# Kernel tuning notes

Measured on AMD Instinct MI355X. Metric: run time of the kernel, lower is better.

The kernel has to match this reference:

```python
import jax, jax.numpy as jnp
import numpy as np

D_MODEL = 1024
H = 16
D_K = D_MODEL // H
NEG_INF = -1.0e9  # matches masked_fill value in the torch source


def setup_inputs() -> dict:
    key = jax.random.key(0)
    kq, kk, kv, kwq, kwk, kwv, kwo = jax.random.split(key, 7)
    B, S = 2, 2048
    query = jax.random.normal(kq, (B, S, D_MODEL), dtype=jnp.float32)
    key_t = jax.random.normal(kk, (B, S, D_MODEL), dtype=jnp.float32)
    value = jax.random.normal(kv, (B, S, D_MODEL), dtype=jnp.float32)
    # causal mask: 1 = attend, 0 = masked (masked_fill(mask == 0, -1e9))
    masked_val = jnp.tril(jnp.ones((S, S), dtype=jnp.int32))[None, None, :, :]
    scale = 1.0 / np.sqrt(D_MODEL)
    w_q = jax.random.normal(kwq, (D_MODEL, D_MODEL), dtype=jnp.float32) * scale
    w_k = jax.random.normal(kwk, (D_MODEL, D_MODEL), dtype=jnp.float32) * scale
    w_v = jax.random.normal(kwv, (D_MODEL, D_MODEL), dtype=jnp.float32) * scale
    w_o = jax.random.normal(kwo, (D_MODEL, D_MODEL), dtype=jnp.float32) * scale
    return {"query": query, "key": key_t, "value": value, "masked_val": masked_val,
            "w_q": w_q, "w_k": w_k, "w_v": w_v, "w_o": w_o}


def reference(query, key, value, masked_val, w_q, w_k, w_v, w_o):
    B, Sq, _ = query.shape
    Sk = key.shape[1]
    # nn.Linear(x) = x @ W.T; weights stored as [out, in]
    Q = (query @ w_q.T).reshape(B, Sq, H, D_K).transpose(0, 2, 1, 3)  # [B,H,Sq,Dk]
    K = (key @ w_k.T).reshape(B, Sk, H, D_K).transpose(0, 2, 1, 3)    # [B,H,Sk,Dk]
    V = (value @ w_v.T).reshape(B, Sk, H, D_K).transpose(0, 2, 1, 3)  # [B,H,Sk,Dk]
    scores = jnp.einsum("bhqd,bhkd->bhqk", Q, K) / jnp.sqrt(jnp.float32(D_K))
    scores = jnp.where(masked_val == 0, NEG_INF, scores)
    probs = jax.nn.softmax(scores, axis=-1)  # dropout p=0.0 -> identity
    ctx = jnp.einsum("bhqk,bhkd->bhqd", probs, V)  # [B,H,Sq,Dk]
    ctx = ctx.transpose(0, 2, 1, 3).reshape(B, Sq, H * D_K)
    return ctx @ w_o.T
```

## Files before the change

### kernel.cpp

```cpp
#include <hip/hip_runtime.h>
#include <hip/hip_bf16.h>
#include <type_traits>

using bf16x8_t = __attribute__((ext_vector_type(8))) __bf16;
using f32x4_t  = __attribute__((ext_vector_type(4))) float;

#define MFMA16(a, b, c) __builtin_amdgcn_mfma_f32_16x16x32_bf16((a), (b), (c), 0, 0, 0)

constexpr int BATCH   = 2;
constexpr int SEQ     = 2048;
constexpr int DMODEL  = 1024;
constexpr int DK      = 64;
constexpr int MTOT    = BATCH * SEQ;
constexpr float SCL2 = 0.125f * 1.44269504088896f;

typedef const __attribute__((address_space(1))) unsigned int ga_u32;
typedef __attribute__((address_space(3))) unsigned int ls_u32;
__device__ __forceinline__ void glds16(const void* g, void* l) {
    __builtin_amdgcn_global_load_lds((ga_u32*)g, (ls_u32*)l, 16, 0, 0);
}

__device__ __forceinline__ float exp2_fast(float x) {
    float r;
    asm volatile("v_exp_f32 %0, %1" : "=v"(r) : "v"(x));
    return r;
}

__device__ __forceinline__ bf16x8_t cvt8(const float* __restrict__ p) {
    f32x4_t a = *(const f32x4_t*)p;
    f32x4_t b = *(const f32x4_t*)(p + 4);
    bf16x8_t r;
    r[0] = (__bf16)a[0]; r[1] = (__bf16)a[1]; r[2] = (__bf16)a[2]; r[3] = (__bf16)a[3];
    r[4] = (__bf16)b[0]; r[5] = (__bf16)b[1]; r[6] = (__bf16)b[2]; r[7] = (__bf16)b[3];
    return r;
}

__global__ __launch_bounds__(256) void cvt_all_kernel(
    const float* __restrict__ q, const float* __restrict__ k, const float* __restrict__ v,
    const float* __restrict__ w0, const float* __restrict__ w1,
    const float* __restrict__ w2, const float* __restrict__ w3,
    __bf16* __restrict__ dstA, __bf16* __restrict__ dstW)
{
    const int y = blockIdx.y;
    const float* src;
    __bf16* dst;
    if (y < 3) {
        const float* a[3] = {q, k, v};
        src = a[y];
        dst = dstA + (size_t)y * (MTOT * DMODEL);
    } else {
        if (blockIdx.x >= 512) return;
        const float* w[4] = {w0, w1, w2, w3};
        src = w[y - 3];
        dst = dstW + (size_t)(y - 3) * (DMODEL * DMODEL);
    }
    size_t i = ((size_t)blockIdx.x * 256 + threadIdx.x) * 8;
    *(bf16x8_t*)(dst + i) = cvt8(src + i);
}

template<bool C_F32>
__device__ __forceinline__ void gemm_body(
    const __bf16* __restrict__ A, const __bf16* __restrict__ Bt,
    void* __restrict__ Cp, int m0, int n0, float cscale)
{
    constexpr int K = DMODEL, N = DMODEL;
    constexpr int NS = K / 32;
    __shared__ __align__(16) char smem[3][16384];

    const int tid  = threadIdx.x;
    const int wave = tid >> 6, lane = tid & 63;
    const int wm = wave >> 1, wn = wave & 1;
    const int l15 = lane & 15, lhi = lane >> 4;

    auto stage = [&](int k0, int buf) {
        #pragma unroll
        for (int i = 0; i < 2; ++i) {
            int cbase = i * 256 + wave * 64;
            int slot = cbase + lane;
            int row = slot >> 2, c = slot & 3;
            int cs = (c + 4 - ((row >> 1) & 3)) & 3;
            glds16(A + (size_t)(m0 + row) * K + k0 + cs * 8, smem[buf] + (size_t)cbase * 16);
        }
        #pragma unroll
        for (int i = 0; i < 2; ++i) {
            int cbase = i * 256 + wave * 64;
            int slot = cbase + lane;
            int row = slot >> 2, c = slot & 3;
            int cs = (c + 4 - ((row >> 1) & 3)) & 3;
            glds16(Bt + (size_t)(n0 + row) * K + k0 + cs * 8,
                   smem[buf] + 8192 + (size_t)cbase * 16);
        }
    };

    f32x4_t acc[4][4] = {};

    auto mfma_step = [&](int buf) {
        const __bf16* a_ls = (const __bf16*)smem[buf];
        const __bf16* b_ls = (const __bf16*)(smem[buf] + 8192);
        bf16x8_t af[4], bfr[4];
        #pragma unroll
        for (int i = 0; i < 4; ++i) {
            int row = wm * 64 + i * 16 + l15;
            int lc = (lhi + (row >> 1)) & 3;
            af[i] = *(const bf16x8_t*)(a_ls + row * 32 + lc * 8);
        }
        #pragma unroll
        for (int j = 0; j < 4; ++j) {
            int row = wn * 64 + j * 16 + l15;
            int lc = (lhi + (row >> 1)) & 3;
            bfr[j] = *(const bf16x8_t*)(b_ls + row * 32 + lc * 8);
        }
        #pragma unroll
        for (int i = 0; i < 4; ++i)
            #pragma unroll
            for (int j = 0; j < 4; ++j)
                acc[i][j] = MFMA16(af[i], bfr[j], acc[i][j]);
    };

    stage(0, 0);
    stage(32, 1);

    for (int t = 0; t < NS - 2; ++t) {
        asm volatile("s_waitcnt vmcnt(4)" ::: "memory");
        __builtin_amdgcn_s_barrier();
        __builtin_amdgcn_sched_barrier(0);
        stage((t + 2) * 32, (t + 2) % 3);
        mfma_step(t % 3);
    }
    asm volatile("s_waitcnt vmcnt(4)" ::: "memory");
    __builtin_amdgcn_s_barrier();
    __builtin_amdgcn_sched_barrier(0);
    mfma_step((NS - 2) % 3);
    asm volatile("s_waitcnt vmcnt(0)" ::: "memory");
    __builtin_amdgcn_s_barrier();
    __builtin_amdgcn_sched_barrier(0);
    mfma_step((NS - 1) % 3);

    #pragma unroll
    for (int i = 0; i < 4; ++i)
        #pragma unroll
        for (int j = 0; j < 4; ++j)
            #pragma unroll
            for (int r = 0; r < 4; ++r) {
                int row = m0 + wm * 64 + i * 16 + lhi * 4 + r;
                int col = n0 + wn * 64 + j * 16 + l15;
                float v = acc[i][j][r] * cscale;
                if constexpr (C_F32)
                    ((float*)Cp)[(size_t)row * N + col] = v;
                else
                    ((__bf16*)Cp)[(size_t)row * N + col] = (__bf16)v;
            }
}

__global__ __launch_bounds__(256) void proj_qkv_kernel(
    const __bf16* __restrict__ act, const __bf16* __restrict__ wc,
    __bf16* __restrict__ oq, __bf16* __restrict__ ok, __bf16* __restrict__ ov)
{
    int lid = blockIdx.x + 8 * blockIdx.y + 256 * blockIdx.z;
    int nid = (lid & 7) * 96 + (lid >> 3);
    int z = nid >> 8, rem = nid & 255;
    int m0 = (rem >> 3) * 128, n0 = (rem & 7) * 128;

    const __bf16* A = act + (size_t)z * (MTOT * DMODEL);
    const __bf16* Bt = wc + (size_t)z * (DMODEL * DMODEL);
    __bf16* C; float cs;
    if (z == 0)      { C = oq; cs = SCL2; }
    else if (z == 1) { C = ok; cs = 1.0f; }
    else             { C = ov; cs = 1.0f; }
    gemm_body<false>(A, Bt, C, m0, n0, cs);
}

__global__ __launch_bounds__(256) void proj_out_kernel(
    const __bf16* __restrict__ ctx, const __bf16* __restrict__ woc, float* __restrict__ out)
{
    int lid = blockIdx.x + 8 * blockIdx.y;
    int nid = (lid & 7) * 32 + (lid >> 3);
    gemm_body<true>(ctx, woc, out, (nid >> 3) * 128, (nid & 7) * 128, 1.0f);
}

__global__ __launch_bounds__(256, 3) void attn_kernel(
    const __bf16* __restrict__ Qm, const __bf16* __restrict__ Km,
    const __bf16* __restrict__ Vm, __bf16* __restrict__ Om)
{
    constexpr int LDV = 72, LDP = 72;
    __shared__ __bf16 k_sh[2][64 * 64];
    __shared__ __bf16 v_sh[2][64 * LDV];
    __shared__ __bf16 p_sh[4][16 * LDP];

    const int tid  = threadIdx.x;
    const int wave = tid >> 6, lane = tid & 63;
    const int l15 = lane & 15, lhi = lane >> 4;

    int old = blockIdx.x + 32 * blockIdx.y;
    int nid = (old & 7) * 128 + (old >> 3);
    const int x = nid & 31, bh = nid >> 5;
    const int p = (bh & 1) ? 31 - x : x;
    const int q0 = p * 64;
    const int b = bh >> 4, h = bh & 15;

    const __bf16* Qb = Qm + (size_t)b * SEQ * DMODEL + h * DK;
    const __bf16* Kb = Km + (size_t)b * SEQ * DMODEL + h * DK;
    const __bf16* Vb = Vm + (size_t)b * SEQ * DMODEL + h * DK;

    const int qbase = q0 + wave * 16;

    bf16x8_t qf[2];
    {
        const __bf16* qp = Qb + (size_t)(qbase + l15) * DMODEL + lhi * 8;
        qf[0] = *(const bf16x8_t*)qp;
        qf[1] = *(const bf16x8_t*)(qp + 32);
    }
    bf16x8_t onesf;
    #pragma unroll
    for (int j = 0; j < 8; ++j) onesf[j] = (__bf16)1.0f;

    f32x4_t acc[4] = {};
    f32x4_t acc_l = {};

    const int vrow = tid >> 3, vgrp = tid & 7;
    bf16x8_t vreg0, vreg1;

    auto stageK = [&](int kv0, int buf) {
        #pragma unroll
        for (int i = 0; i < 2; ++i) {
            int slot = tid + i * 256;
            int row = slot >> 3, c = (slot & 7) ^ (row & 7);
            glds16(Kb + (size_t)(kv0 + row) * DMODEL + c * 8,
                   (char*)k_sh[buf] + (size_t)slot * 16);
        }
    };
    auto loadV = [&](int kv0) {
        vreg0 = *(const bf16x8_t*)(Vb + (size_t)(kv0 + vrow) * DMODEL + vgrp * 8);
        vreg1 = *(const bf16x8_t*)(Vb + (size_t)(kv0 + 32 + vrow) * DMODEL + vgrp * 8);
    };
    auto writeV = [&](int buf) {
        int sh0 = (vrow + vgrp * 8) & 63;
        #pragma unroll
        for (int j = 0; j < 8; ++j) v_sh[buf][(vgrp * 8 + j) * LDV + sh0] = vreg0[j];
        int sh1 = (vrow + 32 + vgrp * 8) & 63;
        #pragma unroll
        for (int j = 0; j < 8; ++j) v_sh[buf][(vgrp * 8 + j) * LDV + sh1] = vreg1[j];
    };

    auto body = [&](auto needmask_c, int kv0, int cur) {
        constexpr bool NEEDMASK = decltype(needmask_c)::value;
        const __bf16* ks_buf = k_sh[cur];
        const __bf16* vs_buf = v_sh[cur];

        f32x4_t sf[4] = {};
        __builtin_amdgcn_s_setprio(1);
        #pragma unroll
        for (int ks = 0; ks < 2; ++ks)
            #pragma unroll
            for (int n = 0; n < 4; ++n) {
                int row = n * 16 + l15;
                bf16x8_t kf = *(const bf16x8_t*)(ks_buf + row * 64 + (((ks * 4 + lhi) ^ (row & 7)) * 8));
                sf[n] = MFMA16(qf[ks], kf, sf[n]);
            }
        __builtin_amdgcn_s_setprio(0);

        const int qrow_base = qbase + lhi * 4;
        #pragma unroll
        for (int r = 0; r < 4; ++r)
            #pragma unroll
            for (int n = 0; n < 4; ++n) {
                float sv = sf[n][r];
                if constexpr (NEEDMASK)
                    if (kv0 + n * 16 + l15 > qrow_base + r) sv = -1.0e30f;
                p_sh[wave][(lhi * 4 + r) * LDP + ((n * 16 + l15 + ((lhi >> 1) << 3)) & 63)]
                    = (__bf16)exp2_fast(sv);
            }

        __builtin_amdgcn_s_setprio(1);
        #pragma unroll
        for (int ks = 0; ks < 2; ++ks) {
            bf16x8_t pa = *(const bf16x8_t*)(
                &p_sh[wave][l15 * LDP + ((ks * 32 + lhi * 8 + ((l15 >> 3) << 3)) & 63)]);
            acc_l = MFMA16(pa, onesf, acc_l);
            #pragma unroll
            for (int n = 0; n < 4; ++n) {
                int d = n * 16 + l15;
                int rot = (ks * 32 + lhi * 8 + ((d >> 3) << 3)) & 63;
                bf16x8_t vf = *(const bf16x8_t*)(vs_buf + d * LDV + rot);
                acc[n] = MFMA16(pa, vf, acc[n]);
            }
        }
        __builtin_amdgcn_s_setprio(0);
    };

    stageK(0, 0);
    loadV(0);
    writeV(0);
    __syncthreads();

    for (int t = 0; t < p; ++t) {
        stageK((t + 1) * 64, (t & 1) ^ 1);
        loadV((t + 1) * 64);
        body(std::integral_constant<bool, false>{}, t * 64, t & 1);
        writeV((t & 1) ^ 1);
        __syncthreads();
    }
    body(std::integral_constant<bool, true>{}, p * 64, p & 1);

    __bf16* Ob = Om + (size_t)b * SEQ * DMODEL + h * DK;
    #pragma unroll
    for (int n = 0; n < 4; ++n)
        #pragma unroll
        for (int r = 0; r < 4; ++r) {
            int row = qbase + lhi * 4 + r;
            Ob[(size_t)row * DMODEL + n * 16 + l15] = (__bf16)(acc[n][r] / acc_l[r]);
        }
}

extern "C" void kernel_launch(void* const* d_in, const int* in_sizes, int n_in,
                              void* d_out, int out_size, void* d_ws, size_t ws_size,
                              hipStream_t stream)
{
    const float* q  = (const float*)d_in[0];
    const float* k  = (const float*)d_in[1];
    const float* v  = (const float*)d_in[2];
    const float* wq = (const float*)d_in[4];
    const float* wk = (const float*)d_in[5];
    const float* wv = (const float*)d_in[6];
    const float* wo = (const float*)d_in[7];
    float* out = (float*)d_out;

    const size_t mat = (size_t)MTOT * DMODEL;
    __bf16* Qw = (__bf16*)d_ws;
    __bf16* Kw = Qw + mat;
    __bf16* Vw = Kw + mat;
    __bf16* Cw = Vw + mat;
    __bf16* Wc = Cw + mat;
    __bf16* Aw = Wc + 4 * (size_t)(DMODEL * DMODEL);

    dim3 blk(256);
    cvt_all_kernel<<<dim3(2048, 7), blk, 0, stream>>>(q, k, v, wq, wk, wv, wo, Aw, Wc);
    proj_qkv_kernel<<<dim3(8, 32, 3), blk, 0, stream>>>(Aw, Wc, Qw, Kw, Vw);
    attn_kernel<<<dim3(32, 32), blk, 0, stream>>>(Qw, Kw, Vw, Cw);
    proj_out_kernel<<<dim3(8, 32), blk, 0, stream>>>(Cw, Wc + 3 * DMODEL * DMODEL, out);
}
```

Baseline: 117.3 us.

## Double attention query tile per block to reuse K/V fragments across two row groups

Each attention block now handles 128 query rows instead of 64, and each wave handles two 16-row sub-tiles. The K and V fragments are loaded from LDS once per KV tile and reused for both sub-tiles, which halves K/V staging traffic per query row. The cost is higher register pressure (launch bounds lowered to 2 blocks per SM), half as many blocks, and coarser causal load balancing. The diagonal handling now processes two masked KV tiles at the end.

```diff
diff --git a/kernel.cpp b/kernel.cpp
--- a/kernel.cpp
+++ b/kernel.cpp
@@ -178,7 +178,7 @@
     gemm_body<true>(ctx, woc, out, (nid >> 3) * 128, (nid & 7) * 128, 1.0f);
 }
 
-__global__ __launch_bounds__(256, 3) void attn_kernel(
+__global__ __launch_bounds__(256, 2) void attn_kernel(
     const __bf16* __restrict__ Qm, const __bf16* __restrict__ Km,
     const __bf16* __restrict__ Vm, __bf16* __restrict__ Om)
 {
@@ -191,31 +191,32 @@
     const int wave = tid >> 6, lane = tid & 63;
     const int l15 = lane & 15, lhi = lane >> 4;
 
-    int old = blockIdx.x + 32 * blockIdx.y;
-    int nid = (old & 7) * 128 + (old >> 3);
-    const int x = nid & 31, bh = nid >> 5;
-    const int p = (bh & 1) ? 31 - x : x;
-    const int q0 = p * 64;
+    int old = blockIdx.x + 16 * blockIdx.y;
+    int nid = (old & 7) * 64 + (old >> 3);
+    const int bh = nid >> 4, x = nid & 15;
+    const int p = ((bh >> 1) & 1) ? 15 - x : x;
+    const int q0 = p * 128;
     const int b = bh >> 4, h = bh & 15;
 
     const __bf16* Qb = Qm + (size_t)b * SEQ * DMODEL + h * DK;
     const __bf16* Kb = Km + (size_t)b * SEQ * DMODEL + h * DK;
     const __bf16* Vb = Vm + (size_t)b * SEQ * DMODEL + h * DK;
 
-    const int qbase = q0 + wave * 16;
-
-    bf16x8_t qf[2];
-    {
-        const __bf16* qp = Qb + (size_t)(qbase + l15) * DMODEL + lhi * 8;
-        qf[0] = *(const bf16x8_t*)qp;
-        qf[1] = *(const bf16x8_t*)(qp + 32);
+    const int qw0 = q0 + wave * 32;
+
+    bf16x8_t qf[2][2];
+    #pragma unroll
+    for (int s = 0; s < 2; ++s) {
+        const __bf16* qp = Qb + (size_t)(qw0 + s * 16 + l15) * DMODEL + lhi * 8;
+        qf[s][0] = *(const bf16x8_t*)qp;
+        qf[s][1] = *(const bf16x8_t*)(qp + 32);
     }
     bf16x8_t onesf;
     #pragma unroll
     for (int j = 0; j < 8; ++j) onesf[j] = (__bf16)1.0f;
 
-    f32x4_t acc[4] = {};
-    f32x4_t acc_l = {};
+    f32x4_t acc[2][4] = {};
+    f32x4_t acc_l[2] = {};
 
     const int vrow = tid >> 3, vgrp = tid & 7;
     bf16x8_t vreg0, vreg1;
@@ -247,45 +248,53 @@
         const __bf16* ks_buf = k_sh[cur];
         const __bf16* vs_buf = v_sh[cur];
 
-        f32x4_t sf[4] = {};
-        __builtin_amdgcn_s_setprio(1);
+        bf16x8_t kf[2][4], vf[2][4];
         #pragma unroll
         for (int ks = 0; ks < 2; ++ks)
             #pragma unroll
             for (int n = 0; n < 4; ++n) {
                 int row = n * 16 + l15;
-                bf16x8_t kf = *(const bf16x8_t*)(ks_buf + row * 64 + (((ks * 4 + lhi) ^ (row & 7)) * 8));
-                sf[n] = MFMA16(qf[ks], kf, sf[n]);
-            }
-        __builtin_amdgcn_s_setprio(0);
-
-        const int qrow_base = qbase + lhi * 4;
-        #pragma unroll
-        for (int r = 0; r < 4; ++r)
-            #pragma unroll
-            for (int n = 0; n < 4; ++n) {
-                float sv = sf[n][r];
-                if constexpr (NEEDMASK)
-                    if (kv0 + n * 16 + l15 > qrow_base + r) sv = -1.0e30f;
-                p_sh[wave][(lhi * 4 + r) * LDP + ((n * 16 + l15 + ((lhi >> 1) << 3)) & 63)]
-                    = (__bf16)exp2_fast(sv);
-            }
-
-        __builtin_amdgcn_s_setprio(1);
-        #pragma unroll
-        for (int ks = 0; ks < 2; ++ks) {
-            bf16x8_t pa = *(const bf16x8_t*)(
-                &p_sh[wave][l15 * LDP + ((ks * 32 + lhi * 8 + ((l15 >> 3) << 3)) & 63)]);
-            acc_l = MFMA16(pa, onesf, acc_l);
-            #pragma unroll
-            for (int n = 0; n < 4; ++n) {
+                kf[ks][n] = *(const bf16x8_t*)(ks_buf + row * 64 + (((ks * 4 + lhi) ^ (row & 7)) * 8));
                 int d = n * 16 + l15;
                 int rot = (ks * 32 + lhi * 8 + ((d >> 3) << 3)) & 63;
-                bf16x8_t vf = *(const bf16x8_t*)(vs_buf + d * LDV + rot);
-                acc[n] = MFMA16(pa, vf, acc[n]);
+                vf[ks][n] = *(const bf16x8_t*)(vs_buf + d * LDV + rot);
             }
-        }
-        __builtin_amdgcn_s_setprio(0);
+
+        #pragma unroll
+        for (int s = 0; s < 2; ++s) {
+            f32x4_t sf[4] = {};
+            __builtin_amdgcn_s_setprio(1);
+            #pragma unroll
+            for (int ks = 0; ks < 2; ++ks)
+                #pragma unroll
+                for (int n = 0; n < 4; ++n)
+                    sf[n] = MFMA16(qf[s][ks], kf[ks][n], sf[n]);
+            __builtin_amdgcn_s_setprio(0);
+
+            const int qrb = qw0 + s * 16 + lhi * 4;
+            #pragma unroll
+            for (int r = 0; r < 4; ++r)
+                #pragma unroll
+                for (int n = 0; n < 4; ++n) {
+                    float sv = sf[n][r];
+                    if constexpr (NEEDMASK)
+                        if (kv0 + n * 16 + l15 > qrb + r) sv = -1.0e30f;
+                    p_sh[wave][(lhi * 4 + r) * LDP + ((n * 16 + l15 + ((lhi >> 1) << 3)) & 63)]
+                        = (__bf16)exp2_fast(sv);
+                }
+
+            __builtin_amdgcn_s_setprio(1);
+            #pragma unroll
+            for (int ks = 0; ks < 2; ++ks) {
+                bf16x8_t pa = *(const bf16x8_t*)(
+                    &p_sh[wave][l15 * LDP + ((ks * 32 + lhi * 8 + ((l15 >> 3) << 3)) & 63)]);
+                acc_l[s] = MFMA16(pa, onesf, acc_l[s]);
+                #pragma unroll
+                for (int n = 0; n < 4; ++n)
+                    acc[s][n] = MFMA16(pa, vf[ks][n], acc[s][n]);
+            }
+            __builtin_amdgcn_s_setprio(0);
+        }
     };
 
     stageK(0, 0);
@@ -293,23 +302,33 @@
     writeV(0);
     __syncthreads();
 
-    for (int t = 0; t < p; ++t) {
+    for (int t = 0; t < 2 * p; ++t) {
         stageK((t + 1) * 64, (t & 1) ^ 1);
         loadV((t + 1) * 64);
         body(std::integral_constant<bool, false>{}, t * 64, t & 1);
         writeV((t & 1) ^ 1);
         __syncthreads();
     }
-    body(std::integral_constant<bool, true>{}, p * 64, p & 1);
+    {
+        const int t = 2 * p;
+        stageK((t + 1) * 64, (t & 1) ^ 1);
+        loadV((t + 1) * 64);
+        body(std::integral_constant<bool, true>{}, t * 64, t & 1);
+        writeV((t & 1) ^ 1);
+        __syncthreads();
+        body(std::integral_constant<bool, true>{}, (t + 1) * 64, (t + 1) & 1);
+    }
 
     __bf16* Ob = Om + (size_t)b * SEQ * DMODEL + h * DK;
     #pragma unroll
-    for (int n = 0; n < 4; ++n)
-        #pragma unroll
-        for (int r = 0; r < 4; ++r) {
-            int row = qbase + lhi * 4 + r;
-            Ob[(size_t)row * DMODEL + n * 16 + l15] = (__bf16)(acc[n][r] / acc_l[r]);
-        }
+    for (int s = 0; s < 2; ++s)
+        #pragma unroll
+        for (int n = 0; n < 4; ++n)
+            #pragma unroll
+            for (int r = 0; r < 4; ++r) {
+                int row = qw0 + s * 16 + lhi * 4 + r;
+                Ob[(size_t)row * DMODEL + n * 16 + l15] = (__bf16)(acc[s][n][r] / acc_l[s][r]);
+            }
 }
 
 extern "C" void kernel_launch(void* const* d_in, const int* in_sizes, int n_in,
@@ -336,6 +355,6 @@
     dim3 blk(256);
     cvt_all_kernel<<<dim3(2048, 7), blk, 0, stream>>>(q, k, v, wq, wk, wv, wo, Aw, Wc);
     proj_qkv_kernel<<<dim3(8, 32, 3), blk, 0, stream>>>(Aw, Wc, Qw, Kw, Vw);
-    attn_kernel<<<dim3(32, 32), blk, 0, stream>>>(Qw, Kw, Vw, Cw);
+    attn_kernel<<<dim3(16, 32), blk, 0, stream>>>(Qw, Kw, Vw, Cw);
     proj_out_kernel<<<dim3(8, 32), blk, 0, stream>>>(Cw, Wc + 3 * DMODEL * DMODEL, out);
 }
```

Result: no change. 116.0 us (-1.1%).
